# Kernel optimization log

Hardware: AMD Instinct MI355X
Metric: run time of the kernel (lower is better)

## Reference

```python
import jax, jax.numpy as jnp
import numpy as np

DT_MIN, DT_MAX = 1e-3, 0.1
DT_RANK, D_STATE = 64, 16


def setup_inputs() -> dict:
    key = jax.random.key(0)
    ks = jax.random.split(key, 8)
    B, L, D_MODEL, D_INNER = 2, 4096, 1024, 2048
    s = 0.02
    return {
        "x": jax.random.normal(ks[0], (B, L, D_MODEL), jnp.float32),
        "W_in": jax.random.normal(ks[1], (D_MODEL, 2 * D_INNER), jnp.float32) * s,
        "W_xproj": jax.random.normal(ks[2], (D_INNER, DT_RANK + 2 * D_STATE), jnp.float32) * s,
        "W_dt": jax.random.normal(ks[3], (DT_RANK, D_INNER), jnp.float32) * s,
        "b_dt": jax.random.normal(ks[4], (D_INNER,), jnp.float32) * s,
        "A_log": jnp.log(jax.random.uniform(ks[5], (D_INNER, D_STATE), jnp.float32) + 0.5),
        "D": jnp.ones((D_INNER,), jnp.float32),
        "W_out": jax.random.normal(ks[6], (D_INNER, D_MODEL), jnp.float32) * s,
    }


def _selective_scan(xp, delta, A, Bm, Cm):
    # xp, delta: [B, L, d_inner]; Bm, Cm: [B, L, d_state]; A: [d_inner, d_state]
    batch, L, d_inner = xp.shape
    d_state = A.shape[1]

    def step(h, inp):
        x_t, dt_t, B_t, C_t = inp  # [B,di], [B,di], [B,ds], [B,ds]
        A_bar = 1.0 + A[None] * dt_t[..., None]            # [B, di, ds]
        B_bar = B_t[:, None, :] * dt_t[..., None]          # [B, di, ds]
        h = A_bar * h + B_bar * x_t[..., None]             # [B, di, ds]
        y_t = jnp.sum(C_t[:, None, :] * h, axis=-1)        # [B, di]
        return h, y_t

    h0 = jnp.zeros((batch, d_inner, d_state), xp.dtype)
    xs = (
        jnp.swapaxes(xp, 0, 1),
        jnp.swapaxes(delta, 0, 1),
        jnp.swapaxes(Bm, 0, 1),
        jnp.swapaxes(Cm, 0, 1),
    )
    _, ys = jax.lax.scan(step, h0, xs)  # ys: [L, B, d_inner]
    return jnp.swapaxes(ys, 0, 1)


def reference(x, W_in, W_xproj, W_dt, b_dt, A_log, D, W_out):
    xz = x @ W_in
    xp, z = jnp.split(xz, 2, axis=-1)                      # [B,L,d_inner] each
    x_dbl = xp @ W_xproj
    dlt, Bm, Cm = jnp.split(x_dbl, [DT_RANK, DT_RANK + D_STATE], axis=-1)
    delta = jnp.clip(jax.nn.softplus(dlt @ W_dt + b_dt), DT_MIN, DT_MAX)
    A = -jnp.exp(A_log)
    y = _selective_scan(xp, delta, A, Bm, Cm)
    y = y + D[None, None, :] * xp
    y = y * jax.nn.silu(z)
    return y @ W_out
```

## Files before the change

kernel.cpp:

```cpp
#include <hip/hip_runtime.h>
#include <cstdint>
#include <cstddef>

typedef unsigned short u16;
typedef __attribute__((ext_vector_type(8))) short bf16x8;
typedef __attribute__((ext_vector_type(4))) float f32x4;

__device__ __forceinline__ float bf2f(u16 u) {
  unsigned v = ((unsigned)u) << 16;
  return __builtin_bit_cast(float, v);
}
__device__ __forceinline__ u16 f2bf(float f) {
  unsigned u = __builtin_bit_cast(unsigned, f);
  u = (u + 0x7FFFu + ((u >> 16) & 1u)) >> 16;
  return (u16)u;
}

__device__ __forceinline__ void gload16(const void* g, void* l) {
  __builtin_amdgcn_global_load_lds(
      (const __attribute__((address_space(1))) void*)g,
      (__attribute__((address_space(3))) void*)l,
      16, 0, 0);
}

__device__ __forceinline__ int swz(int lb) { return lb ^ (((lb >> 9) & 1) << 5); }

__global__ __launch_bounds__(256) void f32_to_bf16_kernel(
    const float* __restrict__ in, u16* __restrict__ out, int n) {
  int i = (blockIdx.x * 256 + threadIdx.x) * 4;
  if (i < n) {
    float4 v = *(const float4*)(in + i);
    ushort4 o;
    o.x = f2bf(v.x); o.y = f2bf(v.y); o.z = f2bf(v.z); o.w = f2bf(v.w);
    *(ushort4*)(out + i) = o;
  }
}

__global__ void transpose_f32_bf16T_kernel(
    const float* __restrict__ in, u16* __restrict__ out, int R, int C) {
  __shared__ float tile[32][33];
  const int bx = blockIdx.x * 32;
  const int by = blockIdx.y * 32;
  const int tx = threadIdx.x, ty = threadIdx.y;
#pragma unroll
  for (int i = 0; i < 32; i += 8)
    tile[ty + i][tx] = in[(size_t)(by + ty + i) * C + bx + tx];
  __syncthreads();
#pragma unroll
  for (int i = 0; i < 32; i += 8)
    out[(size_t)(bx + ty + i) * R + by + tx] = f2bf(tile[tx][ty + i]);
}

template <int BN, int EPI>
__global__ __launch_bounds__(512, 2) void gemm256(
    const u16* __restrict__ Ap, const u16* __restrict__ Btp,
    int M, int N, int K, int gx,
    void* __restrict__ o0, void* __restrict__ o1) {
  constexpr int NFR = BN / 64;
  constexpr int NFH = NFR / 2;
  constexpr int A_ISS = 4;
  constexpr int B_ISS = BN / 64;
  constexpr int WN = BN / 4;
  constexpr int BUFSZ = 32768 + BN * 128;
  __shared__ __align__(1024) char smem[2 * BUFSZ];

  const int tid = threadIdx.x;
  const int wid = tid >> 6, lane = tid & 63;
  const int wr = wid >> 2, wc = wid & 3;
  const int l16 = lane & 15, lk = lane >> 4;

  const int nwg = gridDim.x, bid = blockIdx.x;
  const int rb = (bid & 7) * (nwg >> 3) + (bid >> 3);
  const int bx = rb % gx, by = rb / gx;
  const int m0 = by * 256, n0 = bx * BN;

  const u16* gA[A_ISS];
  const u16* gB[B_ISS];
#pragma unroll
  for (int i = 0; i < A_ISS; ++i) {
    int pb = i * 8192 + tid * 16;
    int lb = swz(pb);
    gA[i] = Ap + (size_t)(m0 + (lb >> 7)) * K + ((lb & 127) >> 1);
  }
#pragma unroll
  for (int i = 0; i < B_ISS; ++i) {
    int pb = i * 8192 + tid * 16;
    int lb = swz(pb);
    gB[i] = Btp + (size_t)(n0 + (lb >> 7)) * K + ((lb & 127) >> 1);
  }

  auto stage = [&](int kt, int bb) {
    char* dst = smem + bb * BUFSZ + (wid << 10);
#pragma unroll
    for (int i = 0; i < A_ISS; ++i)
      gload16(gA[i] + kt * 64, dst + i * 8192);
#pragma unroll
    for (int i = 0; i < B_ISS; ++i)
      gload16(gB[i] + kt * 64, dst + 32768 + i * 8192);
  };

  auto offA = [&](int f, int kk) {
    int lb = (wr * 128 + f * 16 + l16) * 128 + kk * 64 + lk * 16;
    return swz(lb);
  };
  auto offB = [&](int n, int kk) {
    int lb = (wc * WN + n * 16 + l16) * 128 + kk * 64 + lk * 16;
    return swz(lb);
  };

  f32x4 acc[8][NFR];
#pragma unroll
  for (int f = 0; f < 8; ++f)
#pragma unroll
    for (int n = 0; n < NFR; ++n) {
      f32x4 z = {0.f, 0.f, 0.f, 0.f};
      acc[f][n] = z;
    }

  const int NT = K >> 6;
  stage(0, 0);
  stage(1, 1);

  for (int kt = 0; kt < NT; ++kt) {
    const char* bufA = smem + (kt & 1) * BUFSZ;
    const char* bufB = bufA + 32768;
    if (kt < NT - 1) {
      if constexpr (B_ISS == 4) asm volatile("s_waitcnt vmcnt(8)" ::: "memory");
      else                      asm volatile("s_waitcnt vmcnt(6)" ::: "memory");
    } else {
      asm volatile("s_waitcnt vmcnt(0)" ::: "memory");
    }
    __builtin_amdgcn_s_barrier();

    bf16x8 af[4][2], bh[2][NFH][2];
#pragma unroll
    for (int j = 0; j < 4; ++j)
#pragma unroll
      for (int kk = 0; kk < 2; ++kk)
        af[j][kk] = *(const bf16x8*)(bufA + offA(j, kk));
#pragma unroll
    for (int j = 0; j < NFH; ++j)
#pragma unroll
      for (int kk = 0; kk < 2; ++kk)
        bh[0][j][kk] = *(const bf16x8*)(bufB + offB(j, kk));
    __builtin_amdgcn_s_setprio(1);
#pragma unroll
    for (int j = 0; j < 4; ++j)
#pragma unroll
      for (int n2 = 0; n2 < NFH; ++n2)
#pragma unroll
        for (int kk = 0; kk < 2; ++kk)
          acc[j][n2] = __builtin_amdgcn_mfma_f32_16x16x32_bf16(
              af[j][kk], bh[0][n2][kk], acc[j][n2], 0, 0, 0);
    __builtin_amdgcn_s_setprio(0);
#pragma unroll
    for (int j = 0; j < NFH; ++j)
#pragma unroll
      for (int kk = 0; kk < 2; ++kk)
        bh[1][j][kk] = *(const bf16x8*)(bufB + offB(NFH + j, kk));
    __builtin_amdgcn_s_setprio(1);
#pragma unroll
    for (int j = 0; j < 4; ++j)
#pragma unroll
      for (int n2 = 0; n2 < NFH; ++n2)
#pragma unroll
        for (int kk = 0; kk < 2; ++kk)
          acc[j][NFH + n2] = __builtin_amdgcn_mfma_f32_16x16x32_bf16(
              af[j][kk], bh[1][n2][kk], acc[j][NFH + n2], 0, 0, 0);
    __builtin_amdgcn_s_setprio(0);
#pragma unroll
    for (int j = 0; j < 4; ++j)
#pragma unroll
      for (int kk = 0; kk < 2; ++kk)
        af[j][kk] = *(const bf16x8*)(bufA + offA(4 + j, kk));
    __builtin_amdgcn_s_setprio(1);
#pragma unroll
    for (int j = 0; j < 4; ++j)
#pragma unroll
      for (int n2 = 0; n2 < NFH; ++n2)
#pragma unroll
        for (int kk = 0; kk < 2; ++kk)
          acc[4 + j][NFH + n2] = __builtin_amdgcn_mfma_f32_16x16x32_bf16(
              af[j][kk], bh[1][n2][kk], acc[4 + j][NFH + n2], 0, 0, 0);
    __builtin_amdgcn_s_setprio(0);
    __builtin_amdgcn_s_setprio(1);
#pragma unroll
    for (int j = 0; j < 4; ++j)
#pragma unroll
      for (int n2 = 0; n2 < NFH; ++n2)
#pragma unroll
        for (int kk = 0; kk < 2; ++kk)
          acc[4 + j][n2] = __builtin_amdgcn_mfma_f32_16x16x32_bf16(
              af[j][kk], bh[0][n2][kk], acc[4 + j][n2], 0, 0, 0);
    __builtin_amdgcn_s_setprio(0);

    asm volatile("s_waitcnt lgkmcnt(0)" ::: "memory");
    __builtin_amdgcn_s_barrier();
    if (kt + 2 < NT) stage(kt + 2, kt & 1);
  }

#pragma unroll
  for (int f = 0; f < 8; ++f) {
#pragma unroll
    for (int n = 0; n < NFR; ++n) {
#pragma unroll
      for (int rr = 0; rr < 4; ++rr) {
        const int row = m0 + wr * 128 + f * 16 + lk * 4 + rr;
        const int col = n0 + wc * WN + n * 16 + l16;
        float v = acc[f][n][rr];
        if constexpr (EPI == 0) {
          if (col < 2048) {
            ((u16*)o0)[(size_t)row * 2048 + col] = f2bf(v);
          } else {
            float sv = v / (1.f + __expf(-v));
            ((u16*)o1)[(size_t)row * 2048 + (col - 2048)] = f2bf(sv);
          }
        } else {
          ((float*)o0)[(size_t)row * (size_t)N + col] = v;
        }
      }
    }
  }
}

template <int BN, int NR, int EPI>
__global__ __launch_bounds__(256) void gemm_bt(
    const u16* __restrict__ A, const u16* __restrict__ Bt,
    int M, int N, int K,
    void* __restrict__ o0, void* __restrict__ o1, void* __restrict__ o2,
    const float* __restrict__ bias) {
  constexpr int BM = 128, BK = 32, MR = 4;
  __shared__ __align__(16) u16 As[BM * BK];
  __shared__ __align__(16) u16 Bs[BN * BK];
  const int tid = threadIdx.x;
  const int wid = tid >> 6, lane = tid & 63;
  const int wr = wid >> 1, wc = wid & 1;
  const int m0 = blockIdx.y * BM, n0 = blockIdx.x * BN;
  const int l16 = lane & 15, lk = lane >> 4;

  f32x4 acc[MR][NR];
#pragma unroll
  for (int m = 0; m < MR; ++m)
#pragma unroll
    for (int n = 0; n < NR; ++n) {
      f32x4 z = {0.f, 0.f, 0.f, 0.f};
      acc[m][n] = z;
    }

  constexpr int CH_A = (BM * BK * 2) / 1024;
  constexpr int CH_B = (BN * BK * 2) / 1024;

  for (int k0 = 0; k0 < K; k0 += BK) {
    for (int c = wid; c < CH_A; c += 4) {
      int off = c * 1024 + lane * 16;
      int e = off >> 1;
      int m = e >> 5, kk = e & 31;
      gload16(A + (size_t)(m0 + m) * K + (k0 + kk), (char*)As + off);
    }
    for (int c = wid; c < CH_B; c += 4) {
      int off = c * 1024 + lane * 16;
      int e = off >> 1;
      int n = e >> 5, kk = e & 31;
      gload16(Bt + (size_t)(n0 + n) * K + (k0 + kk), (char*)Bs + off);
    }
    __syncthreads();
    bf16x8 af[MR], bfr[NR];
#pragma unroll
    for (int m = 0; m < MR; ++m)
      af[m] = *(const bf16x8*)(As + (wr * 64 + m * 16 + l16) * BK + lk * 8);
#pragma unroll
    for (int n = 0; n < NR; ++n)
      bfr[n] = *(const bf16x8*)(Bs + (wc * (NR * 16) + n * 16 + l16) * BK + lk * 8);
#pragma unroll
    for (int m = 0; m < MR; ++m)
#pragma unroll
      for (int n = 0; n < NR; ++n)
        acc[m][n] = __builtin_amdgcn_mfma_f32_16x16x32_bf16(af[m], bfr[n], acc[m][n], 0, 0, 0);
    __syncthreads();
  }

#pragma unroll
  for (int m = 0; m < MR; ++m) {
#pragma unroll
    for (int n = 0; n < NR; ++n) {
#pragma unroll
      for (int r = 0; r < 4; ++r) {
        const int row = m0 + wr * 64 + m * 16 + (lane >> 4) * 4 + r;
        const int col = n0 + wc * (NR * 16) + n * 16 + (lane & 15);
        float v = acc[m][n][r];
        if constexpr (EPI == 1) {
          if (col < 64) {
            ((u16*)o0)[(size_t)row * 64 + col] = f2bf(v);
          } else if (col < 80) {
            ((float*)o1)[(size_t)row * 16 + (col - 64)] = v;
          } else {
            ((float*)o2)[(size_t)row * 16 + (col - 80)] = v;
          }
        } else if constexpr (EPI == 2) {
          v += bias[col];
          float sp = (v > 20.f) ? v : log1pf(__expf(v));
          sp = fminf(fmaxf(sp, 1e-3f), 0.1f);
          ((u16*)o0)[(size_t)row * 2048 + col] = f2bf(sp);
        }
      }
    }
  }
}

template <int TC>
__global__ __launch_bounds__(256) void scan_pass1(
    const u16* __restrict__ xp, const u16* __restrict__ dt,
    const float* __restrict__ Bc, const float* __restrict__ A_log,
    float* __restrict__ P, float* __restrict__ Q, int NC) {
  const int di = blockIdx.x * 256 + threadIdx.x;
  const int c = blockIdx.y, b = blockIdx.z;
  __shared__ __align__(16) float Bs[TC * 16];
  {
    const float* src = Bc + (size_t)(b * 4096 + c * TC) * 16;
    for (int i = threadIdx.x; i < TC * 4; i += 256)
      *(float4*)(Bs + i * 4) = *(const float4*)(src + i * 4);
  }
  float A[16], h[16], Pp[16];
#pragma unroll
  for (int s = 0; s < 16; ++s) {
    A[s] = -__expf(A_log[di * 16 + s]);
    h[s] = 0.f;
    Pp[s] = 1.f;
  }
  __syncthreads();
  size_t gidx = (size_t)(b * 4096 + c * TC) * 2048 + di;
  for (int t = 0; t < TC; ++t, gidx += 2048) {
    float xv = bf2f(xp[gidx]), dv = bf2f(dt[gidx]);
    float dvx = dv * xv;
#pragma unroll
    for (int q = 0; q < 4; ++q) {
      f32x4 bv = ((const f32x4*)(Bs + t * 16))[q];
#pragma unroll
      for (int j = 0; j < 4; ++j) {
        int s = q * 4 + j;
        float abar = fmaf(A[s], dv, 1.f);
        h[s] = fmaf(abar, h[s], bv[j] * dvx);
        Pp[s] *= abar;
      }
    }
  }
  const size_t obase = ((size_t)(b * NC + c) * 16) * 2048 + di;
#pragma unroll
  for (int s = 0; s < 16; ++s) {
    P[obase + (size_t)s * 2048] = Pp[s];
    Q[obase + (size_t)s * 2048] = h[s];
  }
}

__global__ __launch_bounds__(256) void scan_pass2(
    const float* __restrict__ P, const float* __restrict__ Q,
    float* __restrict__ Hin, int NC) {
  const int di = blockIdx.x * 256 + threadIdx.x;
  const int s = blockIdx.y, b = blockIdx.z;
  float hin = 0.f;
  const size_t idx0 = ((size_t)(b * NC) * 16 + s) * 2048 + di;
#pragma unroll 8
  for (int c = 0; c < NC; ++c) {
    size_t idx = idx0 + (size_t)c * (16 * 2048);
    Hin[idx] = hin;
    hin = fmaf(P[idx], hin, Q[idx]);
  }
}

template <int TC>
__global__ __launch_bounds__(256) void scan_pass3(
    const u16* __restrict__ xp, const u16* __restrict__ dt,
    const u16* __restrict__ zs, const float* __restrict__ Bc,
    const float* __restrict__ Cc, const float* __restrict__ A_log,
    const float* __restrict__ Dv, const float* __restrict__ Hin,
    u16* __restrict__ Y, int NC) {
  const int di = blockIdx.x * 256 + threadIdx.x;
  const int c = blockIdx.y, b = blockIdx.z;
  __shared__ __align__(16) float Bs[TC * 16], Cs[TC * 16];
  {
    const float* srcB = Bc + (size_t)(b * 4096 + c * TC) * 16;
    const float* srcC = Cc + (size_t)(b * 4096 + c * TC) * 16;
    for (int i = threadIdx.x; i < TC * 4; i += 256) {
      *(float4*)(Bs + i * 4) = *(const float4*)(srcB + i * 4);
      *(float4*)(Cs + i * 4) = *(const float4*)(srcC + i * 4);
    }
  }
  float A[16], h[16];
  const size_t hbase = ((size_t)(b * NC + c) * 16) * 2048 + di;
#pragma unroll
  for (int s = 0; s < 16; ++s) {
    A[s] = -__expf(A_log[di * 16 + s]);
    h[s] = Hin[hbase + (size_t)s * 2048];
  }
  const float Dg = Dv[di];
  __syncthreads();
  size_t gidx = (size_t)(b * 4096 + c * TC) * 2048 + di;
  for (int t = 0; t < TC; ++t, gidx += 2048) {
    float xv = bf2f(xp[gidx]), dv = bf2f(dt[gidx]), zv = bf2f(zs[gidx]);
    float dvx = dv * xv;
    float y = 0.f;
#pragma unroll
    for (int q = 0; q < 4; ++q) {
      f32x4 bv = ((const f32x4*)(Bs + t * 16))[q];
      f32x4 cv = ((const f32x4*)(Cs + t * 16))[q];
#pragma unroll
      for (int j = 0; j < 4; ++j) {
        int s = q * 4 + j;
        float abar = fmaf(A[s], dv, 1.f);
        h[s] = fmaf(abar, h[s], bv[j] * dvx);
        y = fmaf(cv[j], h[s], y);
      }
    }
    float yo = fmaf(Dg, xv, y) * zv;
    Y[gidx] = f2bf(yo);
  }
}

extern "C" void kernel_launch(void* const* d_in, const int* in_sizes, int n_in,
                              void* d_out, int out_size, void* d_ws, size_t ws_size,
                              hipStream_t stream) {
  (void)in_sizes; (void)n_in; (void)out_size; (void)ws_size;
  const float* x       = (const float*)d_in[0];
  const float* W_in    = (const float*)d_in[1];
  const float* W_xproj = (const float*)d_in[2];
  const float* W_dt    = (const float*)d_in[3];
  const float* b_dt    = (const float*)d_in[4];
  const float* A_log   = (const float*)d_in[5];
  const float* Dv      = (const float*)d_in[6];
  const float* W_out   = (const float*)d_in[7];
  float* out = (float*)d_out;

  constexpr size_t MB = 1ull << 20;
  char* ws = (char*)d_ws;
  constexpr size_t O_XP    = 0;
  constexpr size_t O_ZS    = 32 * MB;
  constexpr size_t O_DELTA = 64 * MB;
  constexpr size_t O_BC    = 96 * MB;
  constexpr size_t O_CC    = O_BC + 512 * 1024;
  constexpr size_t O_WOUTT = 97 * MB;
  constexpr size_t O_Y     = 101 * MB;
  constexpr size_t O_XB    = 133 * MB;
  constexpr size_t O_WINT  = 149 * MB;
  constexpr size_t O_WXT   = 157 * MB;
  constexpr size_t O_WDTT  = O_WXT + 393216;
  constexpr size_t O_DLT   = O_WDTT + 262144;
  constexpr size_t O_P     = 133 * MB;
  constexpr size_t O_Q     = 149 * MB;
  constexpr size_t O_HIN   = 165 * MB;

  u16* xb    = (u16*)(ws + O_XB);
  u16* WinT  = (u16*)(ws + O_WINT);
  u16* WxT   = (u16*)(ws + O_WXT);
  u16* WdtT  = (u16*)(ws + O_WDTT);
  u16* WoutT = (u16*)(ws + O_WOUTT);
  u16* xpb   = (u16*)(ws + O_XP);
  u16* zsb   = (u16*)(ws + O_ZS);
  u16* dltb  = (u16*)(ws + O_DLT);
  float* Bcf = (float*)(ws + O_BC);
  float* Ccf = (float*)(ws + O_CC);
  u16* delb  = (u16*)(ws + O_DELTA);
  u16* Yb    = (u16*)(ws + O_Y);
  float* Pf  = (float*)(ws + O_P);
  float* Qf  = (float*)(ws + O_Q);
  float* Hin = (float*)(ws + O_HIN);

  dim3 tb(32, 8);
  f32_to_bf16_kernel<<<8192 * 1024 / 1024, 256, 0, stream>>>(x, xb, 8192 * 1024);
  transpose_f32_bf16T_kernel<<<dim3(4096 / 32, 1024 / 32), tb, 0, stream>>>(W_in, WinT, 1024, 4096);
  transpose_f32_bf16T_kernel<<<dim3(96 / 32, 2048 / 32), tb, 0, stream>>>(W_xproj, WxT, 2048, 96);
  transpose_f32_bf16T_kernel<<<dim3(2048 / 32, 64 / 32), tb, 0, stream>>>(W_dt, WdtT, 64, 2048);
  transpose_f32_bf16T_kernel<<<dim3(1024 / 32, 2048 / 32), tb, 0, stream>>>(W_out, WoutT, 2048, 1024);

  gemm256<256, 0><<<512, 512, 0, stream>>>(
      xb, WinT, 8192, 4096, 1024, 16, xpb, zsb);
  gemm_bt<96, 3, 1><<<dim3(1, 8192 / 128), 256, 0, stream>>>(
      xpb, WxT, 8192, 96, 2048, dltb, Bcf, Ccf, nullptr);
  gemm_bt<128, 4, 2><<<dim3(2048 / 128, 8192 / 128), 256, 0, stream>>>(
      dltb, WdtT, 8192, 2048, 64, delb, nullptr, nullptr, b_dt);

  constexpr int NC = 64, TC = 64;
  scan_pass1<TC><<<dim3(8, NC, 2), 256, 0, stream>>>(
      xpb, delb, Bcf, A_log, Pf, Qf, NC);
  scan_pass2<<<dim3(8, 16, 2), 256, 0, stream>>>(Pf, Qf, Hin, NC);
  scan_pass3<TC><<<dim3(8, NC, 2), 256, 0, stream>>>(
      xpb, delb, zsb, Bcf, Ccf, A_log, Dv, Hin, Yb, NC);

  gemm256<128, 3><<<256, 512, 0, stream>>>(
      Yb, WoutT, 8192, 1024, 2048, 8, out, nullptr);
}
```

Measured before the change: 361.1 us.

## Split-K the x_proj GEMM with a reduction kernel and change LDS swizzle

The narrow x_proj GEMM (N=96, K=2048) previously launched only 64 blocks. It now splits K four ways across blockIdx.z, writing fp32 partials that a new reduce kernel sums and scatters into the bf16 dt-low-rank buffer and the fp32 B/C buffers. This raises GPU occupancy at the cost of an extra launch and extra partial-sum traffic. The LDS swizzle function used by the large GEMMs is also changed to an XOR over more address bits, aiming to reduce bank conflicts.

```diff
diff --git a/kernel.cpp b/kernel.cpp
--- a/kernel.cpp
+++ b/kernel.cpp
@@ -23,7 +23,7 @@
       16, 0, 0);
 }
 
-__device__ __forceinline__ int swz(int lb) { return lb ^ (((lb >> 9) & 1) << 5); }
+__device__ __forceinline__ int swz(int lb) { return lb ^ (((lb >> 7) & 7) << 4); }
 
 __global__ __launch_bounds__(256) void f32_to_bf16_kernel(
     const float* __restrict__ in, u16* __restrict__ out, int n) {
@@ -226,9 +226,8 @@
 template <int BN, int NR, int EPI>
 __global__ __launch_bounds__(256) void gemm_bt(
     const u16* __restrict__ A, const u16* __restrict__ Bt,
-    int M, int N, int K,
-    void* __restrict__ o0, void* __restrict__ o1, void* __restrict__ o2,
-    const float* __restrict__ bias) {
+    int M, int N, int K, int KS,
+    void* __restrict__ o0, const float* __restrict__ bias) {
   constexpr int BM = 128, BK = 32, MR = 4;
   __shared__ __align__(16) u16 As[BM * BK];
   __shared__ __align__(16) u16 Bs[BN * BK];
@@ -250,7 +249,8 @@
   constexpr int CH_A = (BM * BK * 2) / 1024;
   constexpr int CH_B = (BN * BK * 2) / 1024;
 
-  for (int k0 = 0; k0 < K; k0 += BK) {
+  const int kbeg = blockIdx.z * KS, kend = kbeg + KS;
+  for (int k0 = kbeg; k0 < kend; k0 += BK) {
     for (int c = wid; c < CH_A; c += 4) {
       int off = c * 1024 + lane * 16;
       int e = off >> 1;
@@ -288,22 +288,38 @@
         const int row = m0 + wr * 64 + m * 16 + (lane >> 4) * 4 + r;
         const int col = n0 + wc * (NR * 16) + n * 16 + (lane & 15);
         float v = acc[m][n][r];
-        if constexpr (EPI == 1) {
-          if (col < 64) {
-            ((u16*)o0)[(size_t)row * 64 + col] = f2bf(v);
-          } else if (col < 80) {
-            ((float*)o1)[(size_t)row * 16 + (col - 64)] = v;
-          } else {
-            ((float*)o2)[(size_t)row * 16 + (col - 80)] = v;
-          }
-        } else if constexpr (EPI == 2) {
+        if constexpr (EPI == 2) {
           v += bias[col];
           float sp = (v > 20.f) ? v : log1pf(__expf(v));
           sp = fminf(fmaxf(sp, 1e-3f), 0.1f);
           ((u16*)o0)[(size_t)row * 2048 + col] = f2bf(sp);
+        } else {
+          ((float*)o0)[((size_t)blockIdx.z * M + row) * 96 + col] = v;
         }
       }
     }
+  }
+}
+
+__global__ __launch_bounds__(256) void reduce_xdbl(
+    const float* __restrict__ part, u16* __restrict__ dlt,
+    float* __restrict__ Bc, float* __restrict__ Cc) {
+  int idx = blockIdx.x * 256 + threadIdx.x;
+  int row = idx / 24, c4 = idx % 24;
+  const float* p = part + (size_t)row * 96 + c4 * 4;
+  f32x4 v = *(const f32x4*)p;
+#pragma unroll
+  for (int z = 1; z < 4; ++z)
+    v += *(const f32x4*)(p + (size_t)z * 8192 * 96);
+  int col = c4 * 4;
+  if (col < 64) {
+    ushort4 o;
+    o.x = f2bf(v[0]); o.y = f2bf(v[1]); o.z = f2bf(v[2]); o.w = f2bf(v[3]);
+    *(ushort4*)(dlt + (size_t)row * 64 + col) = o;
+  } else if (col < 80) {
+    *(f32x4*)(Bc + (size_t)row * 16 + (col - 64)) = v;
+  } else {
+    *(f32x4*)(Cc + (size_t)row * 16 + (col - 80)) = v;
   }
 }
 
@@ -447,6 +463,7 @@
   constexpr size_t O_P     = 133 * MB;
   constexpr size_t O_Q     = 149 * MB;
   constexpr size_t O_HIN   = 165 * MB;
+  constexpr size_t O_XDP   = O_P;
 
   u16* xb    = (u16*)(ws + O_XB);
   u16* WinT  = (u16*)(ws + O_WINT);
@@ -463,6 +480,7 @@
   float* Pf  = (float*)(ws + O_P);
   float* Qf  = (float*)(ws + O_Q);
   float* Hin = (float*)(ws + O_HIN);
+  float* xdp = (float*)(ws + O_XDP);
 
   dim3 tb(32, 8);
   f32_to_bf16_kernel<<<8192 * 1024 / 1024, 256, 0, stream>>>(x, xb, 8192 * 1024);
@@ -473,10 +491,11 @@
 
   gemm256<256, 0><<<512, 512, 0, stream>>>(
       xb, WinT, 8192, 4096, 1024, 16, xpb, zsb);
-  gemm_bt<96, 3, 1><<<dim3(1, 8192 / 128), 256, 0, stream>>>(
-      xpb, WxT, 8192, 96, 2048, dltb, Bcf, Ccf, nullptr);
-  gemm_bt<128, 4, 2><<<dim3(2048 / 128, 8192 / 128), 256, 0, stream>>>(
-      dltb, WdtT, 8192, 2048, 64, delb, nullptr, nullptr, b_dt);
+  gemm_bt<96, 3, 4><<<dim3(1, 8192 / 128, 4), 256, 0, stream>>>(
+      xpb, WxT, 8192, 96, 2048, 512, xdp, nullptr);
+  reduce_xdbl<<<8192 * 24 / 256, 256, 0, stream>>>(xdp, dltb, Bcf, Ccf);
+  gemm_bt<128, 4, 2><<<dim3(2048 / 128, 8192 / 128, 1), 256, 0, stream>>>(
+      dltb, WdtT, 8192, 2048, 64, 64, delb, b_dt);
 
   constexpr int NC = 64, TC = 64;
   scan_pass1<TC><<<dim3(8, NC, 2), 256, 0, stream>>>(
```

After: 328.1 us. 9.1% less time.
